# Optimization experiments

Measured on AMD Instinct MI355X. Metric: run time of the kernel, lower is better.

## Reference

```python
import jax, jax.numpy as jnp
import numpy as np

DEPTH = 2
DIM = 192
HEADS = 6
MLP_RATIO = 4

def _layernorm(x, g, b):
    mu = jnp.mean(x, -1, keepdims=True)
    var = jnp.var(x, -1, keepdims=True)
    return (x - mu) * jax.lax.rsqrt(var + 1e-5) * g + b

def _scanline_order(pos, w):
    # default space-filling curve of space_filling_cluster: horizontal scanlines
    # with alternating direction in each row (boustrophedon order)
    ix = jnp.floor(pos[..., 0]).astype(jnp.int32)
    iy = jnp.floor(pos[..., 1]).astype(jnp.int32)
    key = iy * w + jnp.where(iy % 2 == 1, w - 1 - ix, ix)
    order_idx = jnp.argsort(key, axis=1)      # rank -> token idx (b, n)
    inv_idx = jnp.argsort(order_idx, axis=1)  # token idx -> rank (b, n)
    return order_idx, inv_idx

def setup_inputs():
    key = jax.random.key(0)
    ks = jax.random.split(key, 8)
    b, h, w, m = 4, 128, 128, 64
    n = h * w
    d = DIM
    dff = MLP_RATIO * d
    s = 0.02
    x = jax.random.normal(ks[0], (b, n, d), jnp.float32)
    # token positions: the full h x w grid, randomly permuted per batch element
    ys, xs = jnp.meshgrid(jnp.arange(h), jnp.arange(w), indexing='ij')
    grid = jnp.stack([xs.reshape(-1), ys.reshape(-1)], -1).astype(jnp.float32)
    perm = jax.vmap(lambda kk: jax.random.permutation(kk, n))(jax.random.split(ks[1], b))
    pos = grid[perm]  # (b, n, 2)
    return {
        'x': x, 'pos': pos,
        'ln1_g': jnp.ones((DEPTH, d)), 'ln1_b': jnp.zeros((DEPTH, d)),
        'w_qkv': jax.random.normal(ks[2], (DEPTH, d, 3 * d), jnp.float32) * s,
        'b_qkv': jnp.zeros((DEPTH, 3 * d)),
        'w_proj': jax.random.normal(ks[3], (DEPTH, d, d), jnp.float32) * s,
        'b_proj': jnp.zeros((DEPTH, d)),
        'ln2_g': jnp.ones((DEPTH, d)), 'ln2_b': jnp.zeros((DEPTH, d)),
        'w_fc1': jax.random.normal(ks[4], (DEPTH, d, dff), jnp.float32) * s,
        'b_fc1': jnp.zeros((DEPTH, dff)),
        'w_fc2': jax.random.normal(ks[5], (DEPTH, dff, d), jnp.float32) * s,
        'b_fc2': jnp.zeros((DEPTH, d)),
        'h': h, 'w': w, 'm': m,
    }

def reference(x, pos, ln1_g, ln1_b, w_qkv, b_qkv, w_proj, b_proj,
              ln2_g, ln2_b, w_fc1, b_fc1, w_fc2, b_fc2, h, w, m):
    b, n, d = x.shape
    dh = d // HEADS
    scale = dh ** -0.5
    kc = n // m  # number of clusters (n chosen divisible by m -> all-ones cluster_mask)
    # clustering is computed under no_grad in the original -> stop_gradient
    order_idx, inv_idx = _scanline_order(jax.lax.stop_gradient(pos), w)
    for i in range(DEPTH):
        # --- cluster attention ---
        xn = _layernorm(x, ln1_g[i], ln1_b[i])
        qkv = xn @ w_qkv[i] + b_qkv[i]                                  # (b, n, 3d)
        qkv = jnp.take_along_axis(qkv, order_idx[..., None], axis=1)    # gather into curve order
        qkv = qkv.reshape(b, kc, m, 3, HEADS, dh)
        q = jnp.transpose(qkv[:, :, :, 0], (0, 1, 3, 2, 4))             # (b, kc, H, m, dh)
        kk = jnp.transpose(qkv[:, :, :, 1], (0, 1, 3, 2, 4))
        v = jnp.transpose(qkv[:, :, :, 2], (0, 1, 3, 2, 4))
        att = jax.nn.softmax(jnp.einsum('bkhqd,bkhpd->bkhqp', q, kk) * scale, axis=-1)
        o = jnp.einsum('bkhqp,bkhpd->bkhqd', att, v)
        o = jnp.transpose(o, (0, 1, 3, 2, 4)).reshape(b, n, d)
        o = jnp.take_along_axis(o, inv_idx[..., None], axis=1)          # scatter back to token order
        x = x + o @ w_proj[i] + b_proj[i]
        # --- MLP ---
        yn = _layernorm(x, ln2_g[i], ln2_b[i])
        x = x + jax.nn.gelu(yn @ w_fc1[i] + b_fc1[i]) @ w_fc2[i] + b_fc2[i]
    return x
```

## Files before the change

### kernel.cpp

```cpp
#include <hip/hip_runtime.h>
#include <hip/hip_bf16.h>

typedef __hip_bfloat16 bf16;
typedef __attribute__((ext_vector_type(8))) short short8;
typedef __attribute__((ext_vector_type(4))) short s16x4;
typedef __attribute__((ext_vector_type(4))) float f32x4;

#define B_   4
#define N_   16384
#define D_   192
#define H6   6
#define DH   32
#define MCL  64
#define KC   256
#define DFF  768
#define GW   128
#define MTOK (B_ * N_)

__device__ __forceinline__ bf16 f2b(float x) { return __float2bfloat16(x); }
__device__ __forceinline__ short f2bbits(float x) {
    bf16 h = __float2bfloat16(x); return *(short*)&h;
}

__global__ void zero_out_kernel(float* __restrict__ out, size_t n) {
    size_t i = blockIdx.x * (size_t)blockDim.x + threadIdx.x;
    if (i < n) out[i] = 0.f;
}

__global__ void build_idx(const float* __restrict__ pos, int* __restrict__ order) {
    int tid = blockIdx.x * blockDim.x + threadIdx.x;
    if (tid >= B_ * N_) return;
    int b = tid / N_;
    int ix = (int)floorf(pos[(size_t)tid * 2 + 0]);
    int iy = (int)floorf(pos[(size_t)tid * 2 + 1]);
    int key = iy * GW + ((iy & 1) ? (GW - 1 - ix) : ix);
    key = (int)(((unsigned)key) & (N_ - 1));
    order[(size_t)b * N_ + key] = tid % N_;
}

__global__ void wprep_all(const float* __restrict__ wq, const float* __restrict__ wp,
                          const float* __restrict__ wf1, const float* __restrict__ wf2,
                          bf16* __restrict__ out) {
    int tid = blockIdx.x * blockDim.x + threadIdx.x;
    if (tid >= 2 * 442368) return;
    int l = tid / 442368, r = tid % 442368;
    const float* src; bf16* dst; int K, Nn, e;
    if (r < 110592)      { src = wq  + (size_t)l * 110592; dst = out + (size_t)l * 442368;          K = 192; Nn = 576; e = r; }
    else if (r < 147456) { src = wp  + (size_t)l * 36864;  dst = out + (size_t)l * 442368 + 110592; K = 192; Nn = 192; e = r - 110592; }
    else if (r < 294912) { src = wf1 + (size_t)l * 147456; dst = out + (size_t)l * 442368 + 147456; K = 192; Nn = 768; e = r - 147456; }
    else                 { src = wf2 + (size_t)l * 147456; dst = out + (size_t)l * 442368 + 294912; K = 768; Nn = 192; e = r - 294912; }
    int k = e / Nn, n = e % Nn;
    int idx = ((n >> 4) * (K >> 5) + (k >> 5)) * 512 + (((k >> 3) & 3) * 16 + (n & 15)) * 8 + (k & 7);
    dst[idx] = f2b(src[e]);
}

template<bool GELU>
__global__ __launch_bounds__(256, 4) void gemm_lnk192(
    const float* __restrict__ Ain, const float* __restrict__ lng, const float* __restrict__ lnb,
    const bf16* __restrict__ Wf, const float* __restrict__ bias,
    bf16* __restrict__ Cout, int Nn) {
    __shared__ short Asl[4 * 6 * 512];
    int tid = threadIdx.x;
    int bm = blockIdx.x;
    int w = tid >> 6, lane = tid & 63;
    {
        int r = tid >> 2, qq = tid & 3;
        const float* xr = Ain + ((size_t)(bm * 64) + r) * 192 + qq * 48;
        float4 va[12];
        float s = 0.f, ss = 0.f;
        #pragma unroll
        for (int j = 0; j < 12; j++) {
            va[j] = ((const float4*)xr)[j];
            s  += va[j].x + va[j].y + va[j].z + va[j].w;
            ss += va[j].x * va[j].x + va[j].y * va[j].y + va[j].z * va[j].z + va[j].w * va[j].w;
        }
        s  += __shfl_xor(s, 1);  s  += __shfl_xor(s, 2);
        ss += __shfl_xor(ss, 1); ss += __shfl_xor(ss, 2);
        float mean = s * (1.f / 192.f);
        float var  = ss * (1.f / 192.f) - mean * mean;
        float rs   = rsqrtf(var + 1e-5f);
        const float4* gg = (const float4*)(lng + qq * 48);
        const float4* bb = (const float4*)(lnb + qq * 48);
        #pragma unroll
        for (int j = 0; j < 6; j++) {
            float4 g0 = gg[2 * j], g1 = gg[2 * j + 1], b0 = bb[2 * j], b1 = bb[2 * j + 1];
            float4 x0 = va[2 * j], x1 = va[2 * j + 1];
            short8 o;
            o[0] = f2bbits((x0.x - mean) * rs * g0.x + b0.x);
            o[1] = f2bbits((x0.y - mean) * rs * g0.y + b0.y);
            o[2] = f2bbits((x0.z - mean) * rs * g0.z + b0.z);
            o[3] = f2bbits((x0.w - mean) * rs * g0.w + b0.w);
            o[4] = f2bbits((x1.x - mean) * rs * g1.x + b1.x);
            o[5] = f2bbits((x1.y - mean) * rs * g1.y + b1.y);
            o[6] = f2bbits((x1.z - mean) * rs * g1.z + b1.z);
            o[7] = f2bbits((x1.w - mean) * rs * g1.w + b1.w);
            int k0 = qq * 48 + j * 8;
            int kt = k0 >> 5, qd = (k0 >> 3) & 3;
            *(short8*)&Asl[((r >> 4) * 6 + kt) * 512 + (qd * 16 + (r & 15)) * 8] = o;
        }
    }
    __syncthreads();
    short8 af[6];
    #pragma unroll
    for (int kt = 0; kt < 6; kt++)
        af[kt] = *(short8*)&Asl[(w * 6 + kt) * 512 + lane * 8];
    int quad = lane >> 4, l16 = lane & 15;
    int ntiles = Nn >> 4;
    for (int nt = 0; nt < ntiles; nt++) {
        const short* bp = (const short*)Wf + ((size_t)nt * 6) * 512 + lane * 8;
        f32x4 acc = {};
        #pragma unroll
        for (int kt = 0; kt < 6; kt++) {
            short8 b = *(const short8*)(bp + kt * 512);
            acc = __builtin_amdgcn_mfma_f32_16x16x32_bf16(af[kt], b, acc, 0, 0, 0);
        }
        int col = nt * 16 + l16;
        float bv = bias[col];
        int row0 = bm * 64 + w * 16 + quad * 4;
        #pragma unroll
        for (int rr = 0; rr < 4; rr++) {
            float v = acc[rr] + bv;
            if (GELU) {
                float inner = 0.7978845608028654f * (v + 0.044715f * v * v * v);
                inner = fminf(fmaxf(inner, -12.f), 12.f);
                float e = __expf(2.f * inner);
                v = 0.5f * v * (1.f + (e - 1.f) / (e + 1.f));
            }
            Cout[(size_t)(row0 + rr) * Nn + col] = f2b(v);
        }
    }
}

__global__ __launch_bounds__(256) void gemm_n192(
    const bf16* __restrict__ A, const bf16* __restrict__ Wf, const float* __restrict__ bias,
    const float* __restrict__ Rsrc, float* __restrict__ Rdst, int K) {
    __shared__ short Asl[8 * 6 * 512];
    int tid = threadIdx.x;
    int bm = blockIdx.x;
    int w = tid >> 6, lane = tid & 63;
    int quad = lane >> 4, l16 = lane & 15;
    int nkc = K / 192, ktn = K >> 5;
    int r = tid >> 1, half = tid & 1;
    f32x4 acc[12][2] = {};
    for (int kc = 0; kc < nkc; kc++) {
        if (kc) __syncthreads();
        const short* ar = (const short*)A + ((size_t)(bm * 128) + r) * K + kc * 192 + half * 96;
        #pragma unroll
        for (int j = 0; j < 12; j++) {
            short8 v = *(const short8*)(ar + j * 8);
            int k0 = half * 96 + j * 8;
            int kt = k0 >> 5, qd = (k0 >> 3) & 3;
            *(short8*)&Asl[((r >> 4) * 6 + kt) * 512 + (qd * 16 + (r & 15)) * 8] = v;
        }
        __syncthreads();
        short8 af[2][6];
        #pragma unroll
        for (int mt = 0; mt < 2; mt++)
            #pragma unroll
            for (int kt = 0; kt < 6; kt++)
                af[mt][kt] = *(short8*)&Asl[((w * 2 + mt) * 6 + kt) * 512 + lane * 8];
        #pragma unroll
        for (int nt = 0; nt < 12; nt++) {
            const short* bp = (const short*)Wf + ((size_t)nt * ktn + kc * 6) * 512 + lane * 8;
            #pragma unroll
            for (int kt = 0; kt < 6; kt++) {
                short8 b = *(const short8*)(bp + kt * 512);
                acc[nt][0] = __builtin_amdgcn_mfma_f32_16x16x32_bf16(af[0][kt], b, acc[nt][0], 0, 0, 0);
                acc[nt][1] = __builtin_amdgcn_mfma_f32_16x16x32_bf16(af[1][kt], b, acc[nt][1], 0, 0, 0);
            }
        }
    }
    #pragma unroll
    for (int nt = 0; nt < 12; nt++) {
        int col = nt * 16 + l16;
        float bv = bias[col];
        #pragma unroll
        for (int mt = 0; mt < 2; mt++) {
            int row0 = bm * 128 + (w * 2 + mt) * 16 + quad * 4;
            #pragma unroll
            for (int rr = 0; rr < 4; rr++) {
                size_t idx = (size_t)(row0 + rr) * 192 + col;
                Rdst[idx] = acc[nt][mt][rr] + bv + Rsrc[idx];
            }
        }
    }
}

__global__ __launch_bounds__(256) void mlp_fused(
    const float* __restrict__ Ain, const float* __restrict__ lng, const float* __restrict__ lnb,
    const bf16* __restrict__ W1f, const float* __restrict__ b1,
    const bf16* __restrict__ W2f, const float* __restrict__ b2,
    const float* __restrict__ Rsrc, float* __restrict__ Rdst) {
    __shared__ short Asl[4 * 6 * 512];
    __shared__ short Hsl[4 * 6 * 512];
    int tid = threadIdx.x;
    int bm = blockIdx.x;
    int w = tid >> 6, lane = tid & 63;
    int quad = lane >> 4, l16 = lane & 15;
    {
        int r = tid >> 2, qq = tid & 3;
        const float* xr = Ain + ((size_t)(bm * 64) + r) * 192 + qq * 48;
        float4 va[12];
        float s = 0.f, ss = 0.f;
        #pragma unroll
        for (int j = 0; j < 12; j++) {
            va[j] = ((const float4*)xr)[j];
            s  += va[j].x + va[j].y + va[j].z + va[j].w;
            ss += va[j].x * va[j].x + va[j].y * va[j].y + va[j].z * va[j].z + va[j].w * va[j].w;
        }
        s  += __shfl_xor(s, 1);  s  += __shfl_xor(s, 2);
        ss += __shfl_xor(ss, 1); ss += __shfl_xor(ss, 2);
        float mean = s * (1.f / 192.f);
        float var  = ss * (1.f / 192.f) - mean * mean;
        float rs   = rsqrtf(var + 1e-5f);
        const float4* gg = (const float4*)(lng + qq * 48);
        const float4* bb = (const float4*)(lnb + qq * 48);
        #pragma unroll
        for (int j = 0; j < 6; j++) {
            float4 g0 = gg[2 * j], g1 = gg[2 * j + 1], b0 = bb[2 * j], b1v = bb[2 * j + 1];
            float4 x0 = va[2 * j], x1 = va[2 * j + 1];
            short8 o;
            o[0] = f2bbits((x0.x - mean) * rs * g0.x + b0.x);
            o[1] = f2bbits((x0.y - mean) * rs * g0.y + b0.y);
            o[2] = f2bbits((x0.z - mean) * rs * g0.z + b0.z);
            o[3] = f2bbits((x0.w - mean) * rs * g0.w + b0.w);
            o[4] = f2bbits((x1.x - mean) * rs * g1.x + b1v.x);
            o[5] = f2bbits((x1.y - mean) * rs * g1.y + b1v.y);
            o[6] = f2bbits((x1.z - mean) * rs * g1.z + b1v.z);
            o[7] = f2bbits((x1.w - mean) * rs * g1.w + b1v.w);
            int k0 = qq * 48 + j * 8;
            int kt = k0 >> 5, qd = (k0 >> 3) & 3;
            *(short8*)&Asl[((r >> 4) * 6 + kt) * 512 + (qd * 16 + (r & 15)) * 8] = o;
        }
    }
    __syncthreads();
    f32x4 acc2[3][4] = {};
    for (int qtr = 0; qtr < 4; qtr++) {
        if (qtr) __syncthreads();
        short8 af[4][6];
        #pragma unroll
        for (int mt = 0; mt < 4; mt++)
            #pragma unroll
            for (int kt = 0; kt < 6; kt++)
                af[mt][kt] = *(short8*)&Asl[(mt * 6 + kt) * 512 + lane * 8];
        #pragma unroll
        for (int j = 0; j < 3; j++) {
            int nth = w * 3 + j;
            int ntg = qtr * 12 + nth;
            const short* bp = (const short*)W1f + ((size_t)ntg * 6) * 512 + lane * 8;
            short8 bfr[6];
            #pragma unroll
            for (int kt = 0; kt < 6; kt++) bfr[kt] = *(const short8*)(bp + kt * 512);
            #pragma unroll
            for (int mt = 0; mt < 4; mt++) {
                f32x4 a = {};
                #pragma unroll
                for (int kt = 0; kt < 6; kt++)
                    a = __builtin_amdgcn_mfma_f32_16x16x32_bf16(bfr[kt], af[mt][kt], a, 0, 0, 0);
                int colb = ntg * 16 + quad * 4;
                s16x4 o;
                #pragma unroll
                for (int rr = 0; rr < 4; rr++) {
                    float u = a[rr] + b1[colb + rr];
                    float inner = 0.7978845608028654f * (u + 0.044715f * u * u * u);
                    inner = fminf(fmaxf(inner, -12.f), 12.f);
                    float e = __expf(2.f * inner);
                    o[rr] = f2bbits(0.5f * u * (1.f + (e - 1.f) / (e + 1.f)));
                }
                *(s16x4*)&Hsl[(mt * 6 + (nth >> 1)) * 512
                              + (((nth & 1) * 2 + (quad >> 1)) * 16 + l16) * 8 + (quad & 1) * 4] = o;
            }
        }
        __syncthreads();
        #pragma unroll
        for (int kt = 0; kt < 6; kt++) {
            short8 afh[4];
            #pragma unroll
            for (int mt = 0; mt < 4; mt++)
                afh[mt] = *(short8*)&Hsl[(mt * 6 + kt) * 512 + lane * 8];
            #pragma unroll
            for (int j = 0; j < 3; j++) {
                int nt = w * 3 + j;
                const short* bp = (const short*)W2f + ((size_t)nt * 24 + qtr * 6 + kt) * 512 + lane * 8;
                short8 b = *(const short8*)bp;
                #pragma unroll
                for (int mt = 0; mt < 4; mt++)
                    acc2[j][mt] = __builtin_amdgcn_mfma_f32_16x16x32_bf16(afh[mt], b, acc2[j][mt], 0, 0, 0);
            }
        }
    }
    #pragma unroll
    for (int j = 0; j < 3; j++) {
        int col = (w * 3 + j) * 16 + l16;
        float bv = b2[col];
        #pragma unroll
        for (int mt = 0; mt < 4; mt++) {
            int row0 = bm * 64 + mt * 16 + quad * 4;
            #pragma unroll
            for (int rr = 0; rr < 4; rr++) {
                size_t idx = (size_t)(row0 + rr) * 192 + col;
                Rdst[idx] = acc2[j][mt][rr] + bv + Rsrc[idx];
            }
        }
    }
}

#define PST 72
#define VST 72
#define OST 40
__global__ __launch_bounds__(64) void attn_mfma(const bf16* __restrict__ qkv,
                                                const int* __restrict__ order,
                                                bf16* __restrict__ outb) {
    __shared__ short vT[32 * VST];
    __shared__ short Pl[64 * PST];
    const float scale = 0.17677669529663687f;
    int h = blockIdx.x, c = blockIdx.y, b = blockIdx.z;
    int lane = threadIdx.x;
    int l16 = lane & 15, quad = lane >> 4;
    int t = (int)(((unsigned)order[(size_t)b * N_ + c * MCL + lane]) & (N_ - 1));
    const short* qb = (const short*)qkv + (size_t)b * N_ * 576;
    {
        const short* vp = qb + (size_t)t * 576 + 384 + h * 32;
        short8 v[4];
        #pragma unroll
        for (int i = 0; i < 4; i++) v[i] = *(const short8*)(vp + i * 8);
        #pragma unroll
        for (int i = 0; i < 4; i++)
            #pragma unroll
            for (int e = 0; e < 8; e++)
                vT[(i * 8 + e) * VST + lane] = v[i][e];
    }
    short8 aq[4], bk[4];
    #pragma unroll
    for (int i = 0; i < 4; i++) {
        int tr = __shfl(t, i * 16 + l16);
        const short* rp = qb + (size_t)tr * 576 + h * 32 + quad * 8;
        aq[i] = *(const short8*)rp;
        bk[i] = *(const short8*)(rp + 192);
    }
    f32x4 S[4][4];
    #pragma unroll
    for (int mt = 0; mt < 4; mt++)
        #pragma unroll
        for (int nt = 0; nt < 4; nt++) {
            f32x4 z = {};
            S[mt][nt] = __builtin_amdgcn_mfma_f32_16x16x32_bf16(aq[mt], bk[nt], z, 0, 0, 0);
        }
    __syncthreads();
    #pragma unroll
    for (int mt = 0; mt < 4; mt++)
        #pragma unroll
        for (int r = 0; r < 4; r++) {
            float e0, e1, e2, e3, s;
            float v0 = S[mt][0][r] * scale, v1 = S[mt][1][r] * scale;
            float v2 = S[mt][2][r] * scale, v3 = S[mt][3][r] * scale;
            e0 = __expf(fminf(fmaxf(v0, -30.f), 30.f));
            e1 = __expf(fminf(fmaxf(v1, -30.f), 30.f));
            e2 = __expf(fminf(fmaxf(v2, -30.f), 30.f));
            e3 = __expf(fminf(fmaxf(v3, -30.f), 30.f));
            s = e0 + e1 + e2 + e3;
            s += __shfl_xor(s, 1); s += __shfl_xor(s, 2);
            s += __shfl_xor(s, 4); s += __shfl_xor(s, 8);
            float inv = 1.f / s;
            int row = mt * 16 + quad * 4 + r;
            Pl[row * PST +  0 + l16] = f2bbits(e0 * inv);
            Pl[row * PST + 16 + l16] = f2bbits(e1 * inv);
            Pl[row * PST + 32 + l16] = f2bbits(e2 * inv);
            Pl[row * PST + 48 + l16] = f2bbits(e3 * inv);
        }
    __syncthreads();
    short8 ap[4][2], bv[2][2];
    #pragma unroll
    for (int mt = 0; mt < 4; mt++)
        #pragma unroll
        for (int kt = 0; kt < 2; kt++)
            ap[mt][kt] = *(const short8*)&Pl[(mt * 16 + l16) * PST + kt * 32 + quad * 8];
    #pragma unroll
    for (int nt = 0; nt < 2; nt++)
        #pragma unroll
        for (int kt = 0; kt < 2; kt++)
            bv[nt][kt] = *(const short8*)&vT[(nt * 16 + l16) * VST + kt * 32 + quad * 8];
    f32x4 O[4][2] = {};
    #pragma unroll
    for (int mt = 0; mt < 4; mt++)
        #pragma unroll
        for (int nt = 0; nt < 2; nt++)
            #pragma unroll
            for (int kt = 0; kt < 2; kt++)
                O[mt][nt] = __builtin_amdgcn_mfma_f32_16x16x32_bf16(ap[mt][kt], bv[nt][kt], O[mt][nt], 0, 0, 0);
    __syncthreads();
    short* Ol = Pl;
    #pragma unroll
    for (int mt = 0; mt < 4; mt++) {
        int row = mt * 16 + quad * 4;
        #pragma unroll
        for (int nt = 0; nt < 2; nt++)
            #pragma unroll
            for (int rr = 0; rr < 4; rr++)
                Ol[(row + rr) * OST + nt * 16 + l16] = f2bbits(O[mt][nt][rr]);
    }
    __syncthreads();
    short* op = (short*)outb + ((size_t)b * N_ + t) * 192 + h * 32;
    #pragma unroll
    for (int j = 0; j < 4; j++)
        *(short8*)(op + j * 8) = *(const short8*)&Ol[lane * OST + j * 8];
}

extern "C" void kernel_launch(void* const* d_in, const int* in_sizes, int n_in,
                              void* d_out, int out_size, void* d_ws, size_t ws_size,
                              hipStream_t stream) {
    const float* x_in   = (const float*)d_in[0];
    const float* pos    = (const float*)d_in[1];
    const float* ln1_g  = (const float*)d_in[2];
    const float* ln1_b  = (const float*)d_in[3];
    const float* w_qkv  = (const float*)d_in[4];
    const float* b_qkv  = (const float*)d_in[5];
    const float* w_proj = (const float*)d_in[6];
    const float* b_proj = (const float*)d_in[7];
    const float* ln2_g  = (const float*)d_in[8];
    const float* ln2_b  = (const float*)d_in[9];
    const float* w_fc1  = (const float*)d_in[10];
    const float* b_fc1  = (const float*)d_in[11];
    const float* w_fc2  = (const float*)d_in[12];
    const float* b_fc2  = (const float*)d_in[13];

    size_t sz_x     = (size_t)MTOK * D_ * 4;
    size_t sz_xnob  = (size_t)MTOK * D_ * 2;
    size_t sz_cbuf  = (size_t)MTOK * DFF * 2;
    size_t sz_order = (size_t)B_ * N_ * 4;
    size_t sz_wbuf  = (size_t)2 * 442368 * 2;
    size_t need = sz_x + sz_xnob + sz_cbuf + sz_order + sz_wbuf;
    if (ws_size < need) {
        zero_out_kernel<<<(out_size + 255) / 256, 256, 0, stream>>>((float*)d_out, (size_t)out_size);
        return;
    }
    char* ws = (char*)d_ws;
    float* x_f32 = (float*)ws;  ws += sz_x;
    bf16*  xnob  = (bf16*)ws;   ws += sz_xnob;
    bf16*  cbuf  = (bf16*)ws;   ws += sz_cbuf;
    int*   order = (int*)ws;    ws += sz_order;
    bf16*  wbuf  = (bf16*)ws;   ws += sz_wbuf;

    bf16* wq[2]; bf16* wp[2]; bf16* wf1[2]; bf16* wf2[2];
    for (int l = 0; l < 2; ++l) {
        bf16* p = wbuf + (size_t)l * 442368;
        wq[l]  = p;
        wp[l]  = p + 110592;
        wf1[l] = p + 147456;
        wf2[l] = p + 294912;
    }
    wprep_all<<<(2 * 442368 + 255) / 256, 256, 0, stream>>>(w_qkv, w_proj, w_fc1, w_fc2, wbuf);
    build_idx<<<(B_ * N_ + 255) / 256, 256, 0, stream>>>(pos, order);

    for (int l = 0; l < 2; ++l) {
        const float* xsrc = (l == 0) ? x_in : x_f32;
        float* rdst_mlp = (l == 1) ? (float*)d_out : x_f32;
        gemm_lnk192<false><<<MTOK / 64, 256, 0, stream>>>(
            xsrc, ln1_g + l * D_, ln1_b + l * D_, wq[l], b_qkv + l * 576, cbuf, 576);
        attn_mfma<<<dim3(H6, KC, B_), 64, 0, stream>>>(cbuf, order, xnob);
        gemm_n192<<<MTOK / 128, 256, 0, stream>>>(
            xnob, wp[l], b_proj + l * 192, xsrc, x_f32, 192);
        mlp_fused<<<MTOK / 64, 256, 0, stream>>>(
            x_f32, ln2_g + l * D_, ln2_b + l * D_,
            wf1[l], b_fc1 + l * 768, wf2[l], b_fc2 + l * 192,
            x_f32, rdst_mlp);
    }
}
```

Measured before the change: 532.4 us.

## Fuse projection GEMM with residual into the LayerNorm+MLP kernel

Merges the attention output projection (with bias and residual add) into the MLP kernel, so the post-attention residual stream stays in fp32 shared memory instead of being written to and re-read from global memory. The MLP's final residual is read from shared memory. It also hoists the LN2 A-fragments out of the quarter loop and reuses one shared buffer for the normalized input and the GELU hidden tile. The cost is higher shared-memory use per block (about 74 KB), which may lower occupancy, and the projection now runs on 64-row tiles rather than 128-row tiles.

```diff
diff --git a/kernel.cpp b/kernel.cpp
--- a/kernel.cpp
+++ b/kernel.cpp
@@ -16,6 +16,7 @@
 #define DFF  768
 #define GW   128
 #define MTOK (B_ * N_)
+#define XST  196
 
 __device__ __forceinline__ bf16 f2b(float x) { return __float2bfloat16(x); }
 __device__ __forceinline__ short f2bbits(float x) {
@@ -131,75 +132,65 @@
     }
 }
 
-__global__ __launch_bounds__(256) void gemm_n192(
-    const bf16* __restrict__ A, const bf16* __restrict__ Wf, const float* __restrict__ bias,
-    const float* __restrict__ Rsrc, float* __restrict__ Rdst, int K) {
-    __shared__ short Asl[8 * 6 * 512];
-    int tid = threadIdx.x;
-    int bm = blockIdx.x;
-    int w = tid >> 6, lane = tid & 63;
-    int quad = lane >> 4, l16 = lane & 15;
-    int nkc = K / 192, ktn = K >> 5;
-    int r = tid >> 1, half = tid & 1;
-    f32x4 acc[12][2] = {};
-    for (int kc = 0; kc < nkc; kc++) {
-        if (kc) __syncthreads();
-        const short* ar = (const short*)A + ((size_t)(bm * 128) + r) * K + kc * 192 + half * 96;
-        #pragma unroll
-        for (int j = 0; j < 12; j++) {
-            short8 v = *(const short8*)(ar + j * 8);
-            int k0 = half * 96 + j * 8;
-            int kt = k0 >> 5, qd = (k0 >> 3) & 3;
-            *(short8*)&Asl[((r >> 4) * 6 + kt) * 512 + (qd * 16 + (r & 15)) * 8] = v;
-        }
-        __syncthreads();
-        short8 af[2][6];
-        #pragma unroll
-        for (int mt = 0; mt < 2; mt++)
-            #pragma unroll
-            for (int kt = 0; kt < 6; kt++)
-                af[mt][kt] = *(short8*)&Asl[((w * 2 + mt) * 6 + kt) * 512 + lane * 8];
-        #pragma unroll
-        for (int nt = 0; nt < 12; nt++) {
-            const short* bp = (const short*)Wf + ((size_t)nt * ktn + kc * 6) * 512 + lane * 8;
-            #pragma unroll
-            for (int kt = 0; kt < 6; kt++) {
-                short8 b = *(const short8*)(bp + kt * 512);
-                acc[nt][0] = __builtin_amdgcn_mfma_f32_16x16x32_bf16(af[0][kt], b, acc[nt][0], 0, 0, 0);
-                acc[nt][1] = __builtin_amdgcn_mfma_f32_16x16x32_bf16(af[1][kt], b, acc[nt][1], 0, 0, 0);
-            }
-        }
-    }
-    #pragma unroll
-    for (int nt = 0; nt < 12; nt++) {
-        int col = nt * 16 + l16;
-        float bv = bias[col];
-        #pragma unroll
-        for (int mt = 0; mt < 2; mt++) {
-            int row0 = bm * 128 + (w * 2 + mt) * 16 + quad * 4;
-            #pragma unroll
-            for (int rr = 0; rr < 4; rr++) {
-                size_t idx = (size_t)(row0 + rr) * 192 + col;
-                Rdst[idx] = acc[nt][mt][rr] + bv + Rsrc[idx];
-            }
-        }
-    }
-}
-
-__global__ __launch_bounds__(256) void mlp_fused(
-    const float* __restrict__ Ain, const float* __restrict__ lng, const float* __restrict__ lnb,
+__global__ __launch_bounds__(256) void pm_fused(
+    const bf16* __restrict__ Anob,
+    const bf16* __restrict__ Wpf, const float* __restrict__ bp_,
+    const float* __restrict__ Rsrc,
+    const float* __restrict__ lng, const float* __restrict__ lnb,
     const bf16* __restrict__ W1f, const float* __restrict__ b1,
     const bf16* __restrict__ W2f, const float* __restrict__ b2,
-    const float* __restrict__ Rsrc, float* __restrict__ Rdst) {
-    __shared__ short Asl[4 * 6 * 512];
-    __shared__ short Hsl[4 * 6 * 512];
+    float* __restrict__ Rdst) {
+    __shared__ float Xl[64 * XST];
+    __shared__ short Bsl[4 * 6 * 512];
+    short* Asl = (short*)Xl;
     int tid = threadIdx.x;
     int bm = blockIdx.x;
     int w = tid >> 6, lane = tid & 63;
     int quad = lane >> 4, l16 = lane & 15;
     {
         int r = tid >> 2, qq = tid & 3;
-        const float* xr = Ain + ((size_t)(bm * 64) + r) * 192 + qq * 48;
+        const short* ar = (const short*)Anob + ((size_t)(bm * 64) + r) * 192 + qq * 48;
+        #pragma unroll
+        for (int j = 0; j < 6; j++) {
+            short8 v = *(const short8*)(ar + j * 8);
+            int k0 = qq * 48 + j * 8;
+            int kt = k0 >> 5, qd = (k0 >> 3) & 3;
+            *(short8*)&Asl[((r >> 4) * 6 + kt) * 512 + (qd * 16 + (r & 15)) * 8] = v;
+        }
+    }
+    __syncthreads();
+    short8 afp[6];
+    #pragma unroll
+    for (int kt = 0; kt < 6; kt++)
+        afp[kt] = *(short8*)&Asl[(w * 6 + kt) * 512 + lane * 8];
+    f32x4 acc[12];
+    #pragma unroll
+    for (int nt = 0; nt < 12; nt++) {
+        const short* bp = (const short*)Wpf + ((size_t)nt * 6) * 512 + lane * 8;
+        f32x4 a = {};
+        #pragma unroll
+        for (int kt = 0; kt < 6; kt++) {
+            short8 b = *(const short8*)(bp + kt * 512);
+            a = __builtin_amdgcn_mfma_f32_16x16x32_bf16(afp[kt], b, a, 0, 0, 0);
+        }
+        acc[nt] = a;
+    }
+    __syncthreads();
+    #pragma unroll
+    for (int nt = 0; nt < 12; nt++) {
+        int col = nt * 16 + l16;
+        float bv = bp_[col];
+        int lr0 = w * 16 + quad * 4;
+        #pragma unroll
+        for (int rr = 0; rr < 4; rr++) {
+            float rv = Rsrc[(size_t)(bm * 64 + lr0 + rr) * 192 + col];
+            Xl[(lr0 + rr) * XST + col] = acc[nt][rr] + bv + rv;
+        }
+    }
+    __syncthreads();
+    {
+        int r = tid >> 2, qq = tid & 3;
+        const float* xr = &Xl[r * XST + qq * 48];
         float4 va[12];
         float s = 0.f, ss = 0.f;
         #pragma unroll
@@ -230,19 +221,19 @@
             o[7] = f2bbits((x1.w - mean) * rs * g1.w + b1v.w);
             int k0 = qq * 48 + j * 8;
             int kt = k0 >> 5, qd = (k0 >> 3) & 3;
-            *(short8*)&Asl[((r >> 4) * 6 + kt) * 512 + (qd * 16 + (r & 15)) * 8] = o;
-        }
-    }
-    __syncthreads();
+            *(short8*)&Bsl[((r >> 4) * 6 + kt) * 512 + (qd * 16 + (r & 15)) * 8] = o;
+        }
+    }
+    __syncthreads();
+    short8 af[4][6];
+    #pragma unroll
+    for (int mt = 0; mt < 4; mt++)
+        #pragma unroll
+        for (int kt = 0; kt < 6; kt++)
+            af[mt][kt] = *(short8*)&Bsl[(mt * 6 + kt) * 512 + lane * 8];
     f32x4 acc2[3][4] = {};
     for (int qtr = 0; qtr < 4; qtr++) {
-        if (qtr) __syncthreads();
-        short8 af[4][6];
-        #pragma unroll
-        for (int mt = 0; mt < 4; mt++)
-            #pragma unroll
-            for (int kt = 0; kt < 6; kt++)
-                af[mt][kt] = *(short8*)&Asl[(mt * 6 + kt) * 512 + lane * 8];
+        __syncthreads();
         #pragma unroll
         for (int j = 0; j < 3; j++) {
             int nth = w * 3 + j;
@@ -267,7 +258,7 @@
                     float e = __expf(2.f * inner);
                     o[rr] = f2bbits(0.5f * u * (1.f + (e - 1.f) / (e + 1.f)));
                 }
-                *(s16x4*)&Hsl[(mt * 6 + (nth >> 1)) * 512
+                *(s16x4*)&Bsl[(mt * 6 + (nth >> 1)) * 512
                               + (((nth & 1) * 2 + (quad >> 1)) * 16 + l16) * 8 + (quad & 1) * 4] = o;
             }
         }
@@ -277,7 +268,7 @@
             short8 afh[4];
             #pragma unroll
             for (int mt = 0; mt < 4; mt++)
-                afh[mt] = *(short8*)&Hsl[(mt * 6 + kt) * 512 + lane * 8];
+                afh[mt] = *(short8*)&Bsl[(mt * 6 + kt) * 512 + lane * 8];
             #pragma unroll
             for (int j = 0; j < 3; j++) {
                 int nt = w * 3 + j;
@@ -295,11 +286,11 @@
         float bv = b2[col];
         #pragma unroll
         for (int mt = 0; mt < 4; mt++) {
-            int row0 = bm * 64 + mt * 16 + quad * 4;
+            int lr0 = mt * 16 + quad * 4;
             #pragma unroll
             for (int rr = 0; rr < 4; rr++) {
-                size_t idx = (size_t)(row0 + rr) * 192 + col;
-                Rdst[idx] = acc2[j][mt][rr] + bv + Rsrc[idx];
+                size_t idx = (size_t)(bm * 64 + lr0 + rr) * 192 + col;
+                Rdst[idx] = acc2[j][mt][rr] + bv + Xl[(lr0 + rr) * XST + col];
             }
         }
     }
@@ -454,15 +445,14 @@
 
     for (int l = 0; l < 2; ++l) {
         const float* xsrc = (l == 0) ? x_in : x_f32;
-        float* rdst_mlp = (l == 1) ? (float*)d_out : x_f32;
+        float* rdst = (l == 1) ? (float*)d_out : x_f32;
         gemm_lnk192<false><<<MTOK / 64, 256, 0, stream>>>(
             xsrc, ln1_g + l * D_, ln1_b + l * D_, wq[l], b_qkv + l * 576, cbuf, 576);
         attn_mfma<<<dim3(H6, KC, B_), 64, 0, stream>>>(cbuf, order, xnob);
-        gemm_n192<<<MTOK / 128, 256, 0, stream>>>(
-            xnob, wp[l], b_proj + l * 192, xsrc, x_f32, 192);
-        mlp_fused<<<MTOK / 64, 256, 0, stream>>>(
-            x_f32, ln2_g + l * D_, ln2_b + l * D_,
+        pm_fused<<<MTOK / 64, 256, 0, stream>>>(
+            xnob, wp[l], b_proj + l * 192, xsrc,
+            ln2_g + l * D_, ln2_b + l * D_,
             wf1[l], b_fc1 + l * 768, wf2[l], b_fc2 + l * 192,
-            x_f32, rdst_mlp);
-    }
-}
+            rdst);
+    }
+}
```

Measured after the change: 510.5 us. 1.04x faster.
